# Performance work log

Measured on AMD Instinct MI355X. Metric: run time of the kernel, lower is better.

## Reference

```python
import jax, jax.numpy as jnp
import numpy as np

AGENT_SIZE = 64
NEIGH_SIZE = 64
NUM_HEAD = 4
MID_SIZE = 32
N_AGENT = 200000
HM = NUM_HEAD * MID_SIZE  # 128
OUT = HM // 2             # 64


def _xavier(key, shape):
    fan_in, fan_out = shape[0], shape[1]
    std = (2.0 / (fan_in + fan_out)) ** 0.5
    return jax.random.normal(key, shape, dtype=jnp.float32) * std


def setup_inputs() -> dict:
    key = jax.random.key(0)
    ks = jax.random.split(key, 12)
    agent = jax.random.normal(ks[0], (N_AGENT, AGENT_SIZE), dtype=jnp.float32)
    neighbor = jax.random.normal(ks[1], (N_AGENT, 4, NEIGH_SIZE), dtype=jnp.float32)
    neighbor_mask = jax.random.randint(ks[2], (N_AGENT, 4), 0, 2, dtype=jnp.int32)
    return {
        "agent": agent,
        "neighbor": neighbor,
        "neighbor_mask": neighbor_mask,
        "W_agent": _xavier(ks[3], (AGENT_SIZE, HM)),
        "b_agent": jnp.zeros((HM,), jnp.float32),
        "W_neigh": _xavier(ks[4], (NEIGH_SIZE, HM)),
        "b_neigh": jnp.zeros((HM,), jnp.float32),
        "W_hid": _xavier(ks[5], (NEIGH_SIZE, HM)),
        "b_hid": jnp.zeros((HM,), jnp.float32),
        "W_out": _xavier(ks[6], (HM, OUT)),
        "b_out": jnp.zeros((OUT,), jnp.float32),
    }


def reference(agent, neighbor, neighbor_mask,
              W_agent, b_agent, W_neigh, b_neigh,
              W_hid, b_hid, W_out, b_out):
    n = agent.shape[0]
    mask = neighbor_mask.astype(jnp.float32)  # [n, 4], 1 = masked
    # linear + relu projections
    a = jax.nn.relu(agent @ W_agent + b_agent).reshape(n, NUM_HEAD, MID_SIZE)          # [n,h,m]
    nr = jax.nn.relu(neighbor @ W_neigh + b_neigh).reshape(n, 4, NUM_HEAD, MID_SIZE)   # [n,4,h,m]
    nh = jax.nn.relu(neighbor @ W_hid + b_hid).reshape(n, 4, NUM_HEAD, MID_SIZE)       # [n,4,h,m]
    # attention logits: agent . neighbor per head -> [n, h, 4]
    att = jnp.einsum('nhm,nkhm->nhk', a, nr)
    att_score = jax.nn.softmax(mask[:, None, :] * -1e8 + att, axis=-1)                 # [n,h,4]
    att_score = (1.0 - mask[:, None, :]) * att_score
    # weighted MEAN over the 4 neighbors (faithful to .mean(2))
    out = jnp.einsum('nhk,nkhm->nhm', att_score, nh) / 4.0                              # [n,h,m]
    out = out.reshape(n, HM)
    return jax.nn.relu(out @ W_out + b_out)
```

## Files before the change

kernel.cpp:

```cpp
#include <hip/hip_runtime.h>
#include <cstdint>


typedef _Float16 f16;
typedef f16 f16x8 __attribute__((ext_vector_type(8)));
typedef f16 f16x4 __attribute__((ext_vector_type(4)));
typedef float f32x4 __attribute__((ext_vector_type(4)));

#define MFMA(a, b, c) __builtin_amdgcn_mfma_f32_16x16x32_f16(a, b, c, 0, 0, 0)

__device__ __forceinline__ float rowsum16(float x) {
    x += __int_as_float(__builtin_amdgcn_update_dpp(0, __float_as_int(x), 0x128, 0xf, 0xf, true));
    x += __int_as_float(__builtin_amdgcn_update_dpp(0, __float_as_int(x), 0x124, 0xf, 0xf, true));
    x += __int_as_float(__builtin_amdgcn_update_dpp(0, __float_as_int(x), 0x122, 0xf, 0xf, true));
    x += __int_as_float(__builtin_amdgcn_update_dpp(0, __float_as_int(x), 0x121, 0xf, 0xf, true));
    return x;
}

__global__ void prep_w(const float* __restrict__ Wa, const float* __restrict__ Wn,
                       const float* __restrict__ Wh, const float* __restrict__ Wo,
                       f16* __restrict__ ws) {
    int i = blockIdx.x * 256 + threadIdx.x;
    int m = i >> 13;
    int j = i & 8191;
    if (m < 3) {
        const float* W = (m == 0) ? Wa : ((m == 1) ? Wn : Wh);
        int n = j >> 6, k = j & 63;
        ws[m * 8192 + j] = (f16)W[k * 128 + n];
    } else {
        int n = j >> 7, k = j & 127;
        ws[24576 + j] = (f16)Wo[k * 64 + n];
    }
}

__device__ __forceinline__ int swz(int row, int col) {
    return row * 64 + (col ^ ((row & 7) << 3));
}

__global__ __launch_bounds__(256, 3)
void gat_mfma(const float* __restrict__ agent,
              const float* __restrict__ neighbor,
              const int*   __restrict__ nmask,
              const f16*   __restrict__ ws,
              const float* __restrict__ ba, const float* __restrict__ bn,
              const float* __restrict__ bh, const float* __restrict__ bo,
              float* __restrict__ out)
{
    __shared__ float mneg[256];
    __shared__ f16   sa[16 * 64];
    __shared__ f16   sn[64 * 64];
    __shared__ f16   ot[64 * 136];

    const int tid  = threadIdx.x;
    const int lane = tid & 63;
    const int h    = __builtin_amdgcn_readfirstlane(tid >> 6);
    const int l15  = lane & 15;
    const int q    = lane >> 4;
    const long base = (long)blockIdx.x * 64;

    mneg[tid] = -1e8f * (float)nmask[base * 4 + tid];

    const float bav[2] = { ba[h * 32 + l15], ba[h * 32 + 16 + l15] };
    const float bnv[2] = { bn[h * 32 + l15], bn[h * 32 + 16 + l15] };
    const float bhv[2] = { bh[h * 32 + l15], bh[h * 32 + 16 + l15] };
    const float bov    = bo[h * 16 + l15];

    const f16* wsn = ws + 8192;
    const f16* wsh = ws + 16384;
    const f16* wso = ws + 24576;

    f16x8 wn[2][2], wh[2][2];
    #pragma unroll
    for (int ct = 0; ct < 2; ++ct)
        #pragma unroll
        for (int ks = 0; ks < 2; ++ks) {
            int n = h * 32 + ct * 16 + l15;
            wn[ct][ks] = *(const f16x8*)(wsn + n * 64 + ks * 32 + q * 8);
            wh[ct][ks] = *(const f16x8*)(wsh + n * 64 + ks * 32 + q * 8);
        }

    const int sr  = tid >> 4;
    const int sc4 = (tid & 15) * 4;
    const float* agp = agent    + base * 64;
    const float* nbp = neighbor + base * 4 * 64;

    float4 ra = *(const float4*)(agp + tid * 4);
    float4 rn4[4];
    #pragma unroll
    for (int i = 0; i < 4; ++i)
        rn4[i] = *(const float4*)(nbp + i * 1024 + tid * 4);

    #pragma unroll 1
    for (int rt = 0; rt < 4; ++rt) {
        __syncthreads();

        f16x8 wa[2][2];
        #pragma unroll
        for (int ct = 0; ct < 2; ++ct)
            #pragma unroll
            for (int ks = 0; ks < 2; ++ks)
                wa[ct][ks] = *(const f16x8*)(ws + (h * 32 + ct * 16 + l15) * 64 + ks * 32 + q * 8);

        {
            f16x4 va = { (f16)ra.x, (f16)ra.y, (f16)ra.z, (f16)ra.w };
            *(f16x4*)&sa[swz(sr, sc4)] = va;
            #pragma unroll
            for (int i = 0; i < 4; ++i) {
                int rg = i * 16 + sr;
                int lr = (rg & 3) * 16 + (rg >> 2);
                f16x4 v = { (f16)rn4[i].x, (f16)rn4[i].y, (f16)rn4[i].z, (f16)rn4[i].w };
                *(f16x4*)&sn[swz(lr, sc4)] = v;
            }
        }

        {
            int rtn = (rt < 3) ? rt + 1 : 3;
            ra = *(const float4*)(agp + rtn * 1024 + tid * 4);
            #pragma unroll
            for (int i = 0; i < 4; ++i)
                rn4[i] = *(const float4*)(nbp + rtn * 4096 + i * 1024 + tid * 4);
        }

        __syncthreads();

        f32x4 p0 = { bav[0], bav[0], bav[0], bav[0] };
        f32x4 p1 = { bav[1], bav[1], bav[1], bav[1] };
        {
            f16x8 a0 = *(const f16x8*)&sa[swz(l15, q * 8)];
            f16x8 a1 = *(const f16x8*)&sa[swz(l15, 32 + q * 8)];
            p0 = MFMA(a0, wa[0][0], p0); p0 = MFMA(a1, wa[0][1], p0);
            p1 = MFMA(a0, wa[1][0], p1); p1 = MFMA(a1, wa[1][1], p1);
            #pragma unroll
            for (int r = 0; r < 4; ++r) {
                p0[r] = fmaxf(p0[r], 0.f);
                p1[r] = fmaxf(p1[r], 0.f);
            }
        }

        f32x4 o0 = {0.f, 0.f, 0.f, 0.f}, o1 = {0.f, 0.f, 0.f, 0.f};
        f32x4 ls = {0.f, 0.f, 0.f, 0.f};
        #pragma unroll
        for (int k = 0; k < 4; ++k) {
            int lr = k * 16 + l15;
            f16x8 a0 = *(const f16x8*)&sn[swz(lr, q * 8)];
            f16x8 a1 = *(const f16x8*)&sn[swz(lr, 32 + q * 8)];
            f32x4 n0 = { bnv[0], bnv[0], bnv[0], bnv[0] };
            f32x4 n1 = { bnv[1], bnv[1], bnv[1], bnv[1] };
            f32x4 h0 = { bhv[0], bhv[0], bhv[0], bhv[0] };
            f32x4 h1 = { bhv[1], bhv[1], bhv[1], bhv[1] };
            n0 = MFMA(a0, wn[0][0], n0); n0 = MFMA(a1, wn[0][1], n0);
            n1 = MFMA(a0, wn[1][0], n1); n1 = MFMA(a1, wn[1][1], n1);
            h0 = MFMA(a0, wh[0][0], h0); h0 = MFMA(a1, wh[0][1], h0);
            h1 = MFMA(a0, wh[1][0], h1); h1 = MFMA(a1, wh[1][1], h1);
            #pragma unroll
            for (int r = 0; r < 4; ++r) {
                n0[r] = fmaxf(n0[r], 0.f);
                n1[r] = fmaxf(n1[r], 0.f);
                h0[r] = fmaxf(h0[r], 0.f);
                h1[r] = fmaxf(h1[r], 0.f);
            }
            #pragma unroll
            for (int r = 0; r < 4; ++r) {
                float tp = p0[r] * n0[r] + p1[r] * n1[r];
                float logit = rowsum16(tp);
                float s = logit + mneg[(rt * 16 + q * 4 + r) * 4 + k];
                float e = __expf(s);
                ls[r] += e;
                o0[r] += e * h0[r];
                o1[r] += e * h1[r];
            }
        }

        #pragma unroll
        for (int r = 0; r < 4; ++r) {
            float inv = 0.25f / (ls[r] + 1e-30f);
            int row = rt * 16 + q * 4 + r;
            ot[row * 136 + h * 32 + l15]      = (f16)(o0[r] * inv);
            ot[row * 136 + h * 32 + 16 + l15] = (f16)(o1[r] * inv);
        }
    }
    __syncthreads();

    f16x8 wof[4];
    #pragma unroll
    for (int ks = 0; ks < 4; ++ks)
        wof[ks] = *(const f16x8*)(wso + (h * 16 + l15) * 128 + ks * 32 + q * 8);
    #pragma unroll
    for (int rt = 0; rt < 4; ++rt) {
        f32x4 y = { bov, bov, bov, bov };
        #pragma unroll
        for (int ks = 0; ks < 4; ++ks) {
            f16x8 of = *(const f16x8*)(ot + (rt * 16 + l15) * 136 + ks * 32 + q * 8);
            y = MFMA(of, wof[ks], y);
        }
        #pragma unroll
        for (int r = 0; r < 4; ++r)
            out[(base + rt * 16 + q * 4 + r) * 64 + h * 16 + l15] = fmaxf(y[r], 0.f);
    }
}

extern "C" void kernel_launch(void* const* d_in, const int* in_sizes, int n_in,
                              void* d_out, int out_size, void* d_ws, size_t ws_size,
                              hipStream_t stream) {
    const float* agent    = (const float*)d_in[0];
    const float* neighbor = (const float*)d_in[1];
    const int*   nmask    = (const int*)d_in[2];
    const float* Wa = (const float*)d_in[3];
    const float* ba = (const float*)d_in[4];
    const float* Wn = (const float*)d_in[5];
    const float* bn = (const float*)d_in[6];
    const float* Wh = (const float*)d_in[7];
    const float* bh = (const float*)d_in[8];
    const float* Wo = (const float*)d_in[9];
    const float* bo = (const float*)d_in[10];
    float* out = (float*)d_out;
    f16* ws = (f16*)d_ws;

    prep_w<<<128, 256, 0, stream>>>(Wa, Wn, Wh, Wo, ws);

    const int n = in_sizes[0] / 64;
    const int blocks = n / 64;
    gat_mfma<<<blocks, 256, 0, stream>>>(agent, neighbor, nmask, ws,
                                         ba, bn, bh, bo, out);
}
```

Baseline: 350.0 us.

## Double-buffer LDS staging tiles and hoist agent weight loads out of loop

Measured after the change: 355.0 us. No clear change (+1.4%).

```diff
diff --git a/kernel.cpp b/kernel.cpp
--- a/kernel.cpp
+++ b/kernel.cpp
@@ -47,8 +47,8 @@
               float* __restrict__ out)
 {
     __shared__ float mneg[256];
-    __shared__ f16   sa[16 * 64];
-    __shared__ f16   sn[64 * 64];
+    __shared__ f16   sa[2][16 * 64];
+    __shared__ f16   sn[2][64 * 64];
     __shared__ f16   ot[64 * 136];
 
     const int tid  = threadIdx.x;
@@ -69,12 +69,13 @@
     const f16* wsh = ws + 16384;
     const f16* wso = ws + 24576;
 
-    f16x8 wn[2][2], wh[2][2];
+    f16x8 wa[2][2], wn[2][2], wh[2][2];
     #pragma unroll
     for (int ct = 0; ct < 2; ++ct)
         #pragma unroll
         for (int ks = 0; ks < 2; ++ks) {
             int n = h * 32 + ct * 16 + l15;
+            wa[ct][ks] = *(const f16x8*)(ws  + n * 64 + ks * 32 + q * 8);
             wn[ct][ks] = *(const f16x8*)(wsn + n * 64 + ks * 32 + q * 8);
             wh[ct][ks] = *(const f16x8*)(wsh + n * 64 + ks * 32 + q * 8);
         }
@@ -84,50 +85,42 @@
     const float* agp = agent    + base * 64;
     const float* nbp = neighbor + base * 4 * 64;
 
-    float4 ra = *(const float4*)(agp + tid * 4);
+    {
+        float4 ra = *(const float4*)(agp + tid * 4);
+        float4 rn4[4];
+        #pragma unroll
+        for (int i = 0; i < 4; ++i)
+            rn4[i] = *(const float4*)(nbp + i * 1024 + tid * 4);
+        f16x4 va = { (f16)ra.x, (f16)ra.y, (f16)ra.z, (f16)ra.w };
+        *(f16x4*)&sa[0][swz(sr, sc4)] = va;
+        #pragma unroll
+        for (int i = 0; i < 4; ++i) {
+            int rg = i * 16 + sr;
+            int lr = (rg & 3) * 16 + (rg >> 2);
+            f16x4 v = { (f16)rn4[i].x, (f16)rn4[i].y, (f16)rn4[i].z, (f16)rn4[i].w };
+            *(f16x4*)&sn[0][swz(lr, sc4)] = v;
+        }
+    }
+
+    float4 ra;
     float4 rn4[4];
-    #pragma unroll
-    for (int i = 0; i < 4; ++i)
-        rn4[i] = *(const float4*)(nbp + i * 1024 + tid * 4);
-
     #pragma unroll 1
     for (int rt = 0; rt < 4; ++rt) {
+        const int cur = rt & 1;
         __syncthreads();
 
-        f16x8 wa[2][2];
-        #pragma unroll
-        for (int ct = 0; ct < 2; ++ct)
-            #pragma unroll
-            for (int ks = 0; ks < 2; ++ks)
-                wa[ct][ks] = *(const f16x8*)(ws + (h * 32 + ct * 16 + l15) * 64 + ks * 32 + q * 8);
-
-        {
-            f16x4 va = { (f16)ra.x, (f16)ra.y, (f16)ra.z, (f16)ra.w };
-            *(f16x4*)&sa[swz(sr, sc4)] = va;
-            #pragma unroll
-            for (int i = 0; i < 4; ++i) {
-                int rg = i * 16 + sr;
-                int lr = (rg & 3) * 16 + (rg >> 2);
-                f16x4 v = { (f16)rn4[i].x, (f16)rn4[i].y, (f16)rn4[i].z, (f16)rn4[i].w };
-                *(f16x4*)&sn[swz(lr, sc4)] = v;
-            }
-        }
-
-        {
-            int rtn = (rt < 3) ? rt + 1 : 3;
-            ra = *(const float4*)(agp + rtn * 1024 + tid * 4);
+        if (rt < 3) {
+            ra = *(const float4*)(agp + (rt + 1) * 1024 + tid * 4);
             #pragma unroll
             for (int i = 0; i < 4; ++i)
-                rn4[i] = *(const float4*)(nbp + rtn * 4096 + i * 1024 + tid * 4);
-        }
-
-        __syncthreads();
+                rn4[i] = *(const float4*)(nbp + (rt + 1) * 4096 + i * 1024 + tid * 4);
+        }
 
         f32x4 p0 = { bav[0], bav[0], bav[0], bav[0] };
         f32x4 p1 = { bav[1], bav[1], bav[1], bav[1] };
         {
-            f16x8 a0 = *(const f16x8*)&sa[swz(l15, q * 8)];
-            f16x8 a1 = *(const f16x8*)&sa[swz(l15, 32 + q * 8)];
+            f16x8 a0 = *(const f16x8*)&sa[cur][swz(l15, q * 8)];
+            f16x8 a1 = *(const f16x8*)&sa[cur][swz(l15, 32 + q * 8)];
             p0 = MFMA(a0, wa[0][0], p0); p0 = MFMA(a1, wa[0][1], p0);
             p1 = MFMA(a0, wa[1][0], p1); p1 = MFMA(a1, wa[1][1], p1);
             #pragma unroll
@@ -142,8 +135,8 @@
         #pragma unroll
         for (int k = 0; k < 4; ++k) {
             int lr = k * 16 + l15;
-            f16x8 a0 = *(const f16x8*)&sn[swz(lr, q * 8)];
-            f16x8 a1 = *(const f16x8*)&sn[swz(lr, 32 + q * 8)];
+            f16x8 a0 = *(const f16x8*)&sn[cur][swz(lr, q * 8)];
+            f16x8 a1 = *(const f16x8*)&sn[cur][swz(lr, 32 + q * 8)];
             f32x4 n0 = { bnv[0], bnv[0], bnv[0], bnv[0] };
             f32x4 n1 = { bnv[1], bnv[1], bnv[1], bnv[1] };
             f32x4 h0 = { bhv[0], bhv[0], bhv[0], bhv[0] };
@@ -177,6 +170,18 @@
             int row = rt * 16 + q * 4 + r;
             ot[row * 136 + h * 32 + l15]      = (f16)(o0[r] * inv);
             ot[row * 136 + h * 32 + 16 + l15] = (f16)(o1[r] * inv);
+        }
+
+        if (rt < 3) {
+            f16x4 va = { (f16)ra.x, (f16)ra.y, (f16)ra.z, (f16)ra.w };
+            *(f16x4*)&sa[cur ^ 1][swz(sr, sc4)] = va;
+            #pragma unroll
+            for (int i = 0; i < 4; ++i) {
+                int rg = i * 16 + sr;
+                int lr = (rg & 3) * 16 + (rg >> 2);
+                f16x4 v = { (f16)rn4[i].x, (f16)rn4[i].y, (f16)rn4[i].z, (f16)rn4[i].w };
+                *(f16x4*)&sn[cur ^ 1][swz(lr, sc4)] = v;
+            }
         }
     }
     __syncthreads();
```

## Load whole 64-agent tile upfront into LDS and drop per-subtile barriers

Applied to the files above, without the earlier changes.

After: 357.3 us. +2.1%, slower.

```diff
diff --git a/kernel.cpp b/kernel.cpp
--- a/kernel.cpp
+++ b/kernel.cpp
@@ -37,7 +37,7 @@
     return row * 64 + (col ^ ((row & 7) << 3));
 }
 
-__global__ __launch_bounds__(256, 3)
+__global__ __launch_bounds__(256, 2)
 void gat_mfma(const float* __restrict__ agent,
               const float* __restrict__ neighbor,
               const int*   __restrict__ nmask,
@@ -47,8 +47,8 @@
               float* __restrict__ out)
 {
     __shared__ float mneg[256];
-    __shared__ f16   sa[16 * 64];
-    __shared__ f16   sn[64 * 64];
+    __shared__ f16   sa[64 * 64];
+    __shared__ f16   sn[4 * 64 * 64];
     __shared__ f16   ot[64 * 136];
 
     const int tid  = threadIdx.x;
@@ -58,76 +58,65 @@
     const int q    = lane >> 4;
     const long base = (long)blockIdx.x * 64;
 
-    mneg[tid] = -1e8f * (float)nmask[base * 4 + tid];
+    const float* agp = agent    + base * 64;
+    const float* nbp = neighbor + base * 4 * 64;
+    float4 rA[4];
+    #pragma unroll
+    for (int i = 0; i < 4; ++i)
+        rA[i] = *(const float4*)(agp + i * 1024 + tid * 4);
+    float4 rN[16];
+    #pragma unroll
+    for (int i = 0; i < 16; ++i)
+        rN[i] = *(const float4*)(nbp + i * 1024 + tid * 4);
+    const int mk = nmask[base * 4 + tid];
+
+    const f16* wsn = ws + 8192;
+    const f16* wsh = ws + 16384;
+    const f16* wso = ws + 24576;
+    f16x8 wa[2][2], wn[2][2], wh[2][2];
+    #pragma unroll
+    for (int ct = 0; ct < 2; ++ct)
+        #pragma unroll
+        for (int ks = 0; ks < 2; ++ks) {
+            int n = h * 32 + ct * 16 + l15;
+            wa[ct][ks] = *(const f16x8*)(ws  + n * 64 + ks * 32 + q * 8);
+            wn[ct][ks] = *(const f16x8*)(wsn + n * 64 + ks * 32 + q * 8);
+            wh[ct][ks] = *(const f16x8*)(wsh + n * 64 + ks * 32 + q * 8);
+        }
 
     const float bav[2] = { ba[h * 32 + l15], ba[h * 32 + 16 + l15] };
     const float bnv[2] = { bn[h * 32 + l15], bn[h * 32 + 16 + l15] };
     const float bhv[2] = { bh[h * 32 + l15], bh[h * 32 + 16 + l15] };
     const float bov    = bo[h * 16 + l15];
 
-    const f16* wsn = ws + 8192;
-    const f16* wsh = ws + 16384;
-    const f16* wso = ws + 24576;
-
-    f16x8 wn[2][2], wh[2][2];
-    #pragma unroll
-    for (int ct = 0; ct < 2; ++ct)
-        #pragma unroll
-        for (int ks = 0; ks < 2; ++ks) {
-            int n = h * 32 + ct * 16 + l15;
-            wn[ct][ks] = *(const f16x8*)(wsn + n * 64 + ks * 32 + q * 8);
-            wh[ct][ks] = *(const f16x8*)(wsh + n * 64 + ks * 32 + q * 8);
-        }
+    mneg[tid] = -1e8f * (float)mk;
 
     const int sr  = tid >> 4;
     const int sc4 = (tid & 15) * 4;
-    const float* agp = agent    + base * 64;
-    const float* nbp = neighbor + base * 4 * 64;
-
-    float4 ra = *(const float4*)(agp + tid * 4);
-    float4 rn4[4];
-    #pragma unroll
-    for (int i = 0; i < 4; ++i)
-        rn4[i] = *(const float4*)(nbp + i * 1024 + tid * 4);
+    #pragma unroll
+    for (int i = 0; i < 4; ++i) {
+        f16x4 v = { (f16)rA[i].x, (f16)rA[i].y, (f16)rA[i].z, (f16)rA[i].w };
+        *(f16x4*)&sa[swz(i * 16 + sr, sc4)] = v;
+    }
+    #pragma unroll
+    for (int i = 0; i < 16; ++i) {
+        int rgf = i * 16 + sr;
+        int rt  = rgf >> 6;
+        int rg  = rgf & 63;
+        int lr  = (rg & 3) * 16 + (rg >> 2);
+        f16x4 v = { (f16)rN[i].x, (f16)rN[i].y, (f16)rN[i].z, (f16)rN[i].w };
+        *(f16x4*)&sn[rt * 4096 + swz(lr, sc4)] = v;
+    }
+
+    __syncthreads();
 
     #pragma unroll 1
     for (int rt = 0; rt < 4; ++rt) {
-        __syncthreads();
-
-        f16x8 wa[2][2];
-        #pragma unroll
-        for (int ct = 0; ct < 2; ++ct)
-            #pragma unroll
-            for (int ks = 0; ks < 2; ++ks)
-                wa[ct][ks] = *(const f16x8*)(ws + (h * 32 + ct * 16 + l15) * 64 + ks * 32 + q * 8);
-
-        {
-            f16x4 va = { (f16)ra.x, (f16)ra.y, (f16)ra.z, (f16)ra.w };
-            *(f16x4*)&sa[swz(sr, sc4)] = va;
-            #pragma unroll
-            for (int i = 0; i < 4; ++i) {
-                int rg = i * 16 + sr;
-                int lr = (rg & 3) * 16 + (rg >> 2);
-                f16x4 v = { (f16)rn4[i].x, (f16)rn4[i].y, (f16)rn4[i].z, (f16)rn4[i].w };
-                *(f16x4*)&sn[swz(lr, sc4)] = v;
-            }
-        }
-
-        {
-            int rtn = (rt < 3) ? rt + 1 : 3;
-            ra = *(const float4*)(agp + rtn * 1024 + tid * 4);
-            #pragma unroll
-            for (int i = 0; i < 4; ++i)
-                rn4[i] = *(const float4*)(nbp + rtn * 4096 + i * 1024 + tid * 4);
-        }
-
-        __syncthreads();
-
         f32x4 p0 = { bav[0], bav[0], bav[0], bav[0] };
         f32x4 p1 = { bav[1], bav[1], bav[1], bav[1] };
         {
-            f16x8 a0 = *(const f16x8*)&sa[swz(l15, q * 8)];
-            f16x8 a1 = *(const f16x8*)&sa[swz(l15, 32 + q * 8)];
+            f16x8 a0 = *(const f16x8*)&sa[swz(rt * 16 + l15, q * 8)];
+            f16x8 a1 = *(const f16x8*)&sa[swz(rt * 16 + l15, 32 + q * 8)];
             p0 = MFMA(a0, wa[0][0], p0); p0 = MFMA(a1, wa[0][1], p0);
             p1 = MFMA(a0, wa[1][0], p1); p1 = MFMA(a1, wa[1][1], p1);
             #pragma unroll
@@ -139,11 +128,12 @@
 
         f32x4 o0 = {0.f, 0.f, 0.f, 0.f}, o1 = {0.f, 0.f, 0.f, 0.f};
         f32x4 ls = {0.f, 0.f, 0.f, 0.f};
+        const f16* snt = sn + rt * 4096;
         #pragma unroll
         for (int k = 0; k < 4; ++k) {
             int lr = k * 16 + l15;
-            f16x8 a0 = *(const f16x8*)&sn[swz(lr, q * 8)];
-            f16x8 a1 = *(const f16x8*)&sn[swz(lr, 32 + q * 8)];
+            f16x8 a0 = *(const f16x8*)&snt[swz(lr, q * 8)];
+            f16x8 a1 = *(const f16x8*)&snt[swz(lr, 32 + q * 8)];
             f32x4 n0 = { bnv[0], bnv[0], bnv[0], bnv[0] };
             f32x4 n1 = { bnv[1], bnv[1], bnv[1], bnv[1] };
             f32x4 h0 = { bhv[0], bhv[0], bhv[0], bhv[0] };
```
